# Performance work log

Hardware: AMD Instinct MI355X
Metric: run time of the kernel (lower is better)

Reference implementation:

```python
import jax, jax.numpy as jnp
import numpy as np

NUM_STEPS = 151            # num_steps from __init__
STEP = 2.0 / (NUM_STEPS - 1)
HALF = (NUM_STEPS - 1) // 2  # bin offset: t_j = -1 + j*STEP, 1/STEP = HALF
N = 4096
D = 512
NUM_CLASSES = 751


def _soft_histogram(s, mask, size):
    # Triangular-kernel (linear) soft binning, equivalent to the original
    # indsa/indsb masked-repeat construction: each similarity s in
    # [t_{j-1}, t_j] contributes (1-frac) to bin j-1 and frac to bin j.
    x = s / STEP
    k = jnp.floor(x)           # zero-gradient, plays the role of s_repeat_floor
    frac = x - k               # (s - (t_j - STEP)) / STEP
    kI = k.astype(jnp.int32)
    idx_lo = jnp.clip(kI + HALF, 0, NUM_STEPS - 1)
    idx_hi = jnp.clip(kI + HALF + 1, 0, NUM_STEPS - 1)
    hist = jnp.zeros((NUM_STEPS,), dtype=s.dtype)
    hist = hist.at[idx_lo].add((1.0 - frac) * mask)
    hist = hist.at[idx_hi].add(frac * mask)
    return hist / size


def setup_inputs() -> dict:
    key = jax.random.key(0)
    kf, kc = jax.random.split(key)
    return {
        "features": jax.random.normal(kf, (N, D), dtype=jnp.float32),
        "classes": jax.random.randint(kc, (N,), 0, NUM_CLASSES, dtype=jnp.int32),
    }


def reference(features, classes):
    # L2Normalization
    f = features / jnp.linalg.norm(features, axis=1, keepdims=True)
    dists = f @ f.T                                   # [N, N] cosine sims
    iu, ju = np.triu_indices(features.shape[0], 1)    # static upper-tri pairs
    s = dists[iu, ju]                                 # [P] P = N(N-1)/2
    pos = (classes[iu] == classes[ju]).astype(s.dtype)
    neg = 1.0 - pos
    hist_pos = _soft_histogram(s, pos, jnp.sum(pos))
    hist_neg = _soft_histogram(s, neg, jnp.sum(neg))
    cdf_pos = jnp.cumsum(hist_pos)                    # tril-masked column sums == cumsum
    return jnp.sum(hist_neg * cdf_pos)
```

## Files before the change

kernel.cpp:

```cpp
#include <hip/hip_runtime.h>
#include <math.h>

#define N 4096
#define D 512
#define NUM_STEPS 151
#define HALF_BINS 75
#define INV_STEP 75.0f
#define NUM_CLASSES 751
#define P_TOTAL 8386560.0f

#define WS_SUM_ALL 0
#define WS_POS_CNT 1
#define WS_SUM_POS 2
#define WS_S_POS   3
#define WS_G_OFF   8
#define WS_LIST_OFF 1024
#define MAXP (1 << 18)
#define WS_FEAT_OFF (WS_LIST_OFF + MAXP)
#define WS_FEATB_OFF (WS_FEAT_OFF + N * D)
#define WS_IDX_OFF  (WS_FEATB_OFF + N * D / 2)
#define WS_OFFS_OFF (WS_IDX_OFF + N)
#define WS_POFF_OFF (WS_OFFS_OFF + NUM_CLASSES + 1)

typedef __bf16 bf16x8 __attribute__((ext_vector_type(8)));
typedef float floatx4 __attribute__((ext_vector_type(4)));

__device__ __forceinline__ void load_lds16(const void* g, void* s) {
    __builtin_amdgcn_global_load_lds(
        (const __attribute__((address_space(1))) void*)g,
        (__attribute__((address_space(3))) void*)s, 16, 0, 0);
}

__global__ __launch_bounds__(256) void k_normalize(const float* __restrict__ feat,
                                                   float* __restrict__ nf,
                                                   __bf16* __restrict__ nfb) {
    int row = blockIdx.x;
    int t = threadIdx.x;
    const float* fr = feat + (size_t)row * D;
    float a = fr[t];
    float b = fr[t + 256];
    float ss = a * a + b * b;
    for (int o = 32; o > 0; o >>= 1) ss += __shfl_down(ss, o, 64);
    __shared__ float wsum[4];
    int lane = t & 63, wid = t >> 6;
    if (lane == 0) wsum[wid] = ss;
    __syncthreads();
    float tot = wsum[0] + wsum[1] + wsum[2] + wsum[3];
    float inv = 1.0f / sqrtf(tot);
    float na = a * inv, nb = b * inv;
    nf[(size_t)row * D + t] = na;
    nf[(size_t)row * D + t + 256] = nb;
    nfb[(size_t)row * D + t] = (__bf16)na;
    nfb[(size_t)row * D + t + 256] = (__bf16)nb;
}

__global__ __launch_bounds__(256) void k_sort(const int* __restrict__ cls,
                                              int* __restrict__ rowIdx,
                                              int* __restrict__ offs,
                                              int* __restrict__ pairOffs,
                                              int* __restrict__ posCntOut) {
    __shared__ int hcnt[NUM_CLASSES];
    __shared__ int hoff[NUM_CLASSES];
    __shared__ int poff[NUM_CLASSES];
    __shared__ int wsumR[4], wsumP[4];
    int t = threadIdx.x;
    for (int c = t; c < NUM_CLASSES; c += 256) hcnt[c] = 0;
    __syncthreads();
    for (int n = t; n < N; n += 256) atomicAdd(&hcnt[cls[n]], 1);
    __syncthreads();

    int c0 = t * 3;
    int cntPreR[3], cntPreP[3];
    int myR = 0, myP = 0;
    #pragma unroll
    for (int k = 0; k < 3; ++k) {
        int c = c0 + k;
        int cnt = (c < NUM_CLASSES) ? hcnt[c] : 0;
        cntPreR[k] = myR; cntPreP[k] = myP;
        myR += cnt;
        myP += cnt * (cnt - 1) / 2;
    }
    int lane = t & 63, wv = t >> 6;
    int incR = myR, incP = myP;
    for (int o = 1; o < 64; o <<= 1) {
        int rr = __shfl_up(incR, o, 64);
        int pp = __shfl_up(incP, o, 64);
        if (lane >= o) { incR += rr; incP += pp; }
    }
    if (lane == 63) { wsumR[wv] = incR; wsumP[wv] = incP; }
    __syncthreads();
    int baseR = 0, baseP = 0;
    for (int w = 0; w < wv; ++w) { baseR += wsumR[w]; baseP += wsumP[w]; }
    int exR = baseR + incR - myR;
    int exP = baseP + incP - myP;
    #pragma unroll
    for (int k = 0; k < 3; ++k) {
        int c = c0 + k;
        if (c < NUM_CLASSES) { hoff[c] = exR + cntPreR[k]; poff[c] = exP + cntPreP[k]; }
    }
    __syncthreads();

    for (int c = t; c < NUM_CLASSES; c += 256) hcnt[c] = hoff[c];
    __syncthreads();
    for (int n = t; n < N; n += 256) {
        int p = atomicAdd(&hcnt[cls[n]], 1);
        rowIdx[p] = n;
    }
    for (int c = t; c < NUM_CLASSES; c += 256) { offs[c] = hoff[c]; pairOffs[c] = poff[c]; }
    if (t == 0) {
        int totR = wsumR[0] + wsumR[1] + wsumR[2] + wsumR[3];
        int totP = wsumP[0] + wsumP[1] + wsumP[2] + wsumP[3];
        offs[NUM_CLASSES] = totR;
        pairOffs[NUM_CLASSES] = totP;
        *posCntOut = totP;
    }
}

__global__ __launch_bounds__(256) void k_pospairs3(const float* __restrict__ nf,
                                                   const int* __restrict__ rowIdx,
                                                   const int* __restrict__ offs,
                                                   const int* __restrict__ pairOffs,
                                                   float* __restrict__ posS) {
    int c = blockIdx.x;
    int o0 = offs[c], o1 = offs[c + 1];
    int nc = o1 - o0;
    if (nc < 2) return;
    int nPairs = nc * (nc - 1) / 2;
    int pBase = pairOffs[c];
    int lane = threadIdx.x & 63;
    int wave = threadIdx.x >> 6;
    for (int p = wave; p < nPairs; p += 4) {
        int a = 0, rem = p;
        while (rem >= nc - 1 - a) { rem -= nc - 1 - a; ++a; }
        int b = a + 1 + rem;
        int ri = rowIdx[o0 + a], rj = rowIdx[o0 + b];
        const float4* x4 = (const float4*)(nf + (size_t)ri * D);
        const float4* y4 = (const float4*)(nf + (size_t)rj * D);
        float4 xa = x4[lane * 2], xb = x4[lane * 2 + 1];
        float4 ya = y4[lane * 2], yb = y4[lane * 2 + 1];
        float s = xa.x * ya.x + xa.y * ya.y + xa.z * ya.z + xa.w * ya.w
                + xb.x * yb.x + xb.y * yb.y + xb.z * yb.z + xb.w * yb.w;
        for (int o = 32; o > 0; o >>= 1) s += __shfl_down(s, o, 64);
        if (lane == 0) posS[pBase + p] = s;
    }
}

__global__ __launch_bounds__(256) void k_build_cdf(const float* __restrict__ posS,
                                                   const int* __restrict__ posCnt,
                                                   float* __restrict__ G,
                                                   float* __restrict__ sumPosOut,
                                                   float* __restrict__ sPosOut) {
    __shared__ float hist[NUM_STEPS];
    __shared__ float Gs[NUM_STEPS];
    int t = threadIdx.x;
    int C = *posCnt;
    if (C > MAXP) C = MAXP;
    for (int b = t; b < NUM_STEPS; b += 256) hist[b] = 0.f;
    __syncthreads();
    for (int p = t; p < C; p += 256) {
        float s = posS[p];
        float x = s * INV_STEP;
        float kf = floorf(x);
        float frac = x - kf;
        int kI = (int)kf;
        int lo = min(max(kI + HALF_BINS, 0), NUM_STEPS - 1);
        int hi = min(max(kI + HALF_BINS + 1, 0), NUM_STEPS - 1);
        atomicAdd(&hist[lo], 1.0f - frac);
        atomicAdd(&hist[hi], frac);
    }
    __syncthreads();
    if (t == 0) {
        float invC = (C > 0) ? (1.0f / (float)C) : 0.f;
        float acc = 0.f;
        for (int b = 0; b < NUM_STEPS; ++b) {
            acc += hist[b];
            Gs[b] = acc * invC;
        }
    }
    __syncthreads();
    for (int b = t; b < NUM_STEPS; b += 256) G[b] = Gs[b];
    float ps = 0.f;
    for (int p = t; p < C; p += 256) {
        float s = posS[p];
        float x = s * INV_STEP;
        float kf = floorf(x);
        float frac = x - kf;
        int kI = (int)kf;
        int lo = min(max(kI + HALF_BINS, 0), NUM_STEPS - 1);
        int hi = min(max(kI + HALF_BINS + 1, 0), NUM_STEPS - 1);
        ps += (1.f - frac) * Gs[lo] + frac * Gs[hi];
    }
    for (int o = 32; o > 0; o >>= 1) ps += __shfl_down(ps, o, 64);
    __shared__ float wsum[4];
    int lane = t & 63, wid = t >> 6;
    if (lane == 0) wsum[wid] = ps;
    __syncthreads();
    if (t == 0) {
        *sumPosOut = wsum[0] + wsum[1] + wsum[2] + wsum[3];
        *sPosOut = (float)C;
    }
}

#define TILES_1D 32

__global__ __launch_bounds__(256) void k_gram(const __bf16* __restrict__ nfb,
                                              const float* __restrict__ G,
                                              float* __restrict__ sumAll) {
    int bid = blockIdx.x;
    int ti = 0, rem = bid;
    while (rem >= TILES_1D - ti) { rem -= TILES_1D - ti; ++ti; }
    int tj = ti + rem;

    __shared__ __align__(16) __bf16 As[8 * 512];
    __shared__ __align__(16) __bf16 Bs[8 * 512];
    __shared__ float Gs[NUM_STEPS];

    int tid = threadIdx.x;
    for (int b = tid; b < NUM_STEPS; b += 256) Gs[b] = G[b];

    int lane = tid & 63;
    int wave = tid >> 6;
    int rowA0 = ti * 128, rowB0 = tj * 128;

    int fr2 = lane & 15, kc2 = lane >> 4;
    int pS0 = wave * 2, pS1 = wave * 2 + 1;
    const __bf16* gA0 = nfb + (size_t)(rowA0 + pS0 * 16 + fr2) * D + kc2 * 8;
    const __bf16* gA1 = nfb + (size_t)(rowA0 + pS1 * 16 + fr2) * D + kc2 * 8;
    const __bf16* gB0 = nfb + (size_t)(rowB0 + pS0 * 16 + fr2) * D + kc2 * 8;
    const __bf16* gB1 = nfb + (size_t)(rowB0 + pS1 * 16 + fr2) * D + kc2 * 8;
    __bf16* lA0 = &As[pS0 * 512];
    __bf16* lA1 = &As[pS1 * 512];
    __bf16* lB0 = &Bs[pS0 * 512];
    __bf16* lB1 = &Bs[pS1 * 512];

    int pbA = (wave >> 1) * 4;
    int pbB = (wave & 1) * 4;

    floatx4 acc[4][4] = {};

    for (int kb = 0; kb < D / 32; ++kb) {
        int kbase = kb * 32;
        load_lds16(gA0 + kbase, lA0);
        load_lds16(gA1 + kbase, lA1);
        load_lds16(gB0 + kbase, lB0);
        load_lds16(gB1 + kbase, lB1);
        __syncthreads();

        bf16x8 a[4], b[4];
        #pragma unroll
        for (int r = 0; r < 4; ++r)
            a[r] = *(const bf16x8*)(&As[(pbA + r) * 512 + lane * 8]);
        #pragma unroll
        for (int c = 0; c < 4; ++c)
            b[c] = *(const bf16x8*)(&Bs[(pbB + c) * 512 + lane * 8]);

        #pragma unroll
        for (int r = 0; r < 4; ++r)
            #pragma unroll
            for (int c = 0; c < 4; ++c)
                acc[r][c] = __builtin_amdgcn_mfma_f32_16x16x32_bf16(a[r], b[c], acc[r][c], 0, 0, 0);
        __syncthreads();
    }

    int crow = (lane >> 4) * 4;
    int ccol = lane & 15;
    int wm = pbA * 16, wn = pbB * 16;
    float gsum = 0.f;
    #pragma unroll
    for (int r = 0; r < 4; ++r) {
        #pragma unroll
        for (int c = 0; c < 4; ++c) {
            #pragma unroll
            for (int reg = 0; reg < 4; ++reg) {
                int gi = rowA0 + wm + r * 16 + crow + reg;
                int gj = rowB0 + wn + c * 16 + ccol;
                if (gi < gj) {
                    float s = acc[r][c][reg];
                    float x = s * INV_STEP;
                    float kf = floorf(x);
                    float frac = x - kf;
                    int kI = (int)kf;
                    int lo = min(max(kI + HALF_BINS, 0), NUM_STEPS - 1);
                    int hi = min(max(kI + HALF_BINS + 1, 0), NUM_STEPS - 1);
                    gsum += (1.f - frac) * Gs[lo] + frac * Gs[hi];
                }
            }
        }
    }
    for (int o = 32; o > 0; o >>= 1) gsum += __shfl_down(gsum, o, 64);
    __shared__ float wsum[4];
    if ((tid & 63) == 0) wsum[tid >> 6] = gsum;
    __syncthreads();
    if (tid == 0) atomicAdd(sumAll, wsum[0] + wsum[1] + wsum[2] + wsum[3]);
}

__global__ void k_final(const float* __restrict__ wsf, float* __restrict__ out) {
    float C = wsf[WS_S_POS];
    float sneg = P_TOTAL - C;
    out[0] = (wsf[WS_SUM_ALL] - wsf[WS_SUM_POS]) / sneg;
}

extern "C" void kernel_launch(void* const* d_in, const int* in_sizes, int n_in,
                              void* d_out, int out_size, void* d_ws, size_t ws_size,
                              hipStream_t stream) {
    const float* feat = (const float*)d_in[0];
    const int* cls = (const int*)d_in[1];
    float* out = (float*)d_out;
    float* wsf = (float*)d_ws;
    int* wsi = (int*)d_ws;

    hipMemsetAsync(d_ws, 0, 4096, stream);

    float* nf = wsf + WS_FEAT_OFF;
    __bf16* nfb = (__bf16*)(wsf + WS_FEATB_OFF);
    float* posS = wsf + WS_LIST_OFF;
    float* G = wsf + WS_G_OFF;
    int* rowIdx = wsi + WS_IDX_OFF;
    int* offs = wsi + WS_OFFS_OFF;
    int* pairOffs = wsi + WS_POFF_OFF;

    k_normalize<<<N, 256, 0, stream>>>(feat, nf, nfb);
    k_sort<<<1, 256, 0, stream>>>(cls, rowIdx, offs, pairOffs, wsi + WS_POS_CNT);
    k_pospairs3<<<NUM_CLASSES, 256, 0, stream>>>(nf, rowIdx, offs, pairOffs, posS);
    k_build_cdf<<<1, 256, 0, stream>>>(posS, wsi + WS_POS_CNT, G,
                                       wsf + WS_SUM_POS, wsf + WS_S_POS);
    int nTiles = TILES_1D * (TILES_1D + 1) / 2;
    k_gram<<<nTiles, 256, 0, stream>>>(nfb, G, wsf + WS_SUM_ALL);
    k_final<<<1, 1, 0, stream>>>(wsf, out);
}
```

Baseline: 166.6 us.

## Fuse normalize and sort, precompute pair list, deepen gram K tile, fold final

Merges normalization and class sorting into one launch, with an extra block that builds an explicit list of positive pair row indices. The positive-pair dot-product kernel then reads that list through a flat grid-stride loop and no longer decodes pair indices per class. The gram kernel now stages K=64 per LDS round, halving barrier count, and the final scalar is computed by the last tile through an atomic done counter, which removes the k_final launch. The single-thread-per-class pair enumeration in the sort block may be serial and slow for large classes.

```diff
diff --git a/kernel.cpp b/kernel.cpp
--- a/kernel.cpp
+++ b/kernel.cpp
@@ -8,19 +8,20 @@
 #define INV_STEP 75.0f
 #define NUM_CLASSES 751
 #define P_TOTAL 8386560.0f
+#define TILES_1D 32
+#define NTILES (TILES_1D * (TILES_1D + 1) / 2)
 
 #define WS_SUM_ALL 0
 #define WS_POS_CNT 1
 #define WS_SUM_POS 2
 #define WS_S_POS   3
+#define WS_DONE    4
 #define WS_G_OFF   8
 #define WS_LIST_OFF 1024
 #define MAXP (1 << 18)
-#define WS_FEAT_OFF (WS_LIST_OFF + MAXP)
+#define WS_PAIR_OFF (WS_LIST_OFF + MAXP)
+#define WS_FEAT_OFF (WS_PAIR_OFF + 2 * MAXP)
 #define WS_FEATB_OFF (WS_FEAT_OFF + N * D)
-#define WS_IDX_OFF  (WS_FEATB_OFF + N * D / 2)
-#define WS_OFFS_OFF (WS_IDX_OFF + N)
-#define WS_POFF_OFF (WS_OFFS_OFF + NUM_CLASSES + 1)
 
 typedef __bf16 bf16x8 __attribute__((ext_vector_type(8)));
 typedef float floatx4 __attribute__((ext_vector_type(4)));
@@ -31,39 +32,42 @@
         (__attribute__((address_space(3))) void*)s, 16, 0, 0);
 }
 
-__global__ __launch_bounds__(256) void k_normalize(const float* __restrict__ feat,
-                                                   float* __restrict__ nf,
-                                                   __bf16* __restrict__ nfb) {
-    int row = blockIdx.x;
+__global__ __launch_bounds__(256) void k_prep(const float* __restrict__ feat,
+                                              const int* __restrict__ cls,
+                                              float* __restrict__ nf,
+                                              __bf16* __restrict__ nfb,
+                                              int2* __restrict__ pairRows,
+                                              int* __restrict__ posCntOut,
+                                              float* __restrict__ sPosOut) {
+    __shared__ int shmem[NUM_CLASSES * 3 + N / 4];
+    __shared__ int wsumR[4], wsumP[4];
+    __shared__ float wsumF[4];
     int t = threadIdx.x;
-    const float* fr = feat + (size_t)row * D;
-    float a = fr[t];
-    float b = fr[t + 256];
-    float ss = a * a + b * b;
-    for (int o = 32; o > 0; o >>= 1) ss += __shfl_down(ss, o, 64);
-    __shared__ float wsum[4];
-    int lane = t & 63, wid = t >> 6;
-    if (lane == 0) wsum[wid] = ss;
-    __syncthreads();
-    float tot = wsum[0] + wsum[1] + wsum[2] + wsum[3];
-    float inv = 1.0f / sqrtf(tot);
-    float na = a * inv, nb = b * inv;
-    nf[(size_t)row * D + t] = na;
-    nf[(size_t)row * D + t + 256] = nb;
-    nfb[(size_t)row * D + t] = (__bf16)na;
-    nfb[(size_t)row * D + t + 256] = (__bf16)nb;
-}
-
-__global__ __launch_bounds__(256) void k_sort(const int* __restrict__ cls,
-                                              int* __restrict__ rowIdx,
-                                              int* __restrict__ offs,
-                                              int* __restrict__ pairOffs,
-                                              int* __restrict__ posCntOut) {
-    __shared__ int hcnt[NUM_CLASSES];
-    __shared__ int hoff[NUM_CLASSES];
-    __shared__ int poff[NUM_CLASSES];
-    __shared__ int wsumR[4], wsumP[4];
-    int t = threadIdx.x;
+
+    if (blockIdx.x < N) {
+        int row = blockIdx.x;
+        const float* fr = feat + (size_t)row * D;
+        float a = fr[t];
+        float b = fr[t + 256];
+        float ss = a * a + b * b;
+        for (int o = 32; o > 0; o >>= 1) ss += __shfl_down(ss, o, 64);
+        int lane = t & 63, wid = t >> 6;
+        if (lane == 0) wsumF[wid] = ss;
+        __syncthreads();
+        float tot = wsumF[0] + wsumF[1] + wsumF[2] + wsumF[3];
+        float inv = 1.0f / sqrtf(tot);
+        float na = a * inv, nb = b * inv;
+        nf[(size_t)row * D + t] = na;
+        nf[(size_t)row * D + t + 256] = nb;
+        nfb[(size_t)row * D + t] = (__bf16)na;
+        nfb[(size_t)row * D + t + 256] = (__bf16)nb;
+        return;
+    }
+
+    int* hcnt = shmem;
+    int* hoff = shmem + NUM_CLASSES;
+    int* poff = shmem + 2 * NUM_CLASSES;
+    __shared__ int rowIdxL[N / 2];
     for (int c = t; c < NUM_CLASSES; c += 256) hcnt[c] = 0;
     __syncthreads();
     for (int n = t; n < N; n += 256) atomicAdd(&hcnt[cls[n]], 1);
@@ -104,52 +108,61 @@
     __syncthreads();
     for (int n = t; n < N; n += 256) {
         int p = atomicAdd(&hcnt[cls[n]], 1);
-        rowIdx[p] = n;
-    }
-    for (int c = t; c < NUM_CLASSES; c += 256) { offs[c] = hoff[c]; pairOffs[c] = poff[c]; }
+        int word = p >> 1, sh = (p & 1) * 16;
+        atomicAnd(&rowIdxL[word], ~(0xFFFF << sh));
+        atomicOr(&rowIdxL[word], (n & 0xFFFF) << sh);
+    }
+    __syncthreads();
+
+    for (int c = t; c < NUM_CLASSES; c += 256) {
+        int o0 = hoff[c];
+        int nc = (c + 1 < NUM_CLASSES ? hoff[c + 1]
+                                      : wsumR[0] + wsumR[1] + wsumR[2] + wsumR[3]) - o0;
+        int pb = poff[c];
+        int idx = 0;
+        for (int a = 0; a < nc - 1; ++a) {
+            int sa = o0 + a;
+            int ra = (rowIdxL[sa >> 1] >> ((sa & 1) * 16)) & 0xFFFF;
+            for (int b = a + 1; b < nc; ++b) {
+                int sb = o0 + b;
+                int rb = (rowIdxL[sb >> 1] >> ((sb & 1) * 16)) & 0xFFFF;
+                pairRows[pb + idx] = make_int2(ra, rb);
+                ++idx;
+            }
+        }
+    }
     if (t == 0) {
-        int totR = wsumR[0] + wsumR[1] + wsumR[2] + wsumR[3];
         int totP = wsumP[0] + wsumP[1] + wsumP[2] + wsumP[3];
-        offs[NUM_CLASSES] = totR;
-        pairOffs[NUM_CLASSES] = totP;
         *posCntOut = totP;
-    }
-}
-
-__global__ __launch_bounds__(256) void k_pospairs3(const float* __restrict__ nf,
-                                                   const int* __restrict__ rowIdx,
-                                                   const int* __restrict__ offs,
-                                                   const int* __restrict__ pairOffs,
+        *sPosOut = (float)totP;
+    }
+}
+
+__global__ __launch_bounds__(256) void k_pospairs4(const float* __restrict__ nf,
+                                                   const int2* __restrict__ pairRows,
+                                                   const int* __restrict__ posCnt,
                                                    float* __restrict__ posS) {
-    int c = blockIdx.x;
-    int o0 = offs[c], o1 = offs[c + 1];
-    int nc = o1 - o0;
-    if (nc < 2) return;
-    int nPairs = nc * (nc - 1) / 2;
-    int pBase = pairOffs[c];
+    int nP = *posCnt;
+    if (nP > MAXP) nP = MAXP;
+    int gw = (blockIdx.x * 256 + threadIdx.x) >> 6;
     int lane = threadIdx.x & 63;
-    int wave = threadIdx.x >> 6;
-    for (int p = wave; p < nPairs; p += 4) {
-        int a = 0, rem = p;
-        while (rem >= nc - 1 - a) { rem -= nc - 1 - a; ++a; }
-        int b = a + 1 + rem;
-        int ri = rowIdx[o0 + a], rj = rowIdx[o0 + b];
-        const float4* x4 = (const float4*)(nf + (size_t)ri * D);
-        const float4* y4 = (const float4*)(nf + (size_t)rj * D);
+    for (int p = gw; p < nP; p += 4096) {
+        int2 pr = pairRows[p];
+        const float4* x4 = (const float4*)(nf + (size_t)pr.x * D);
+        const float4* y4 = (const float4*)(nf + (size_t)pr.y * D);
         float4 xa = x4[lane * 2], xb = x4[lane * 2 + 1];
         float4 ya = y4[lane * 2], yb = y4[lane * 2 + 1];
         float s = xa.x * ya.x + xa.y * ya.y + xa.z * ya.z + xa.w * ya.w
                 + xb.x * yb.x + xb.y * yb.y + xb.z * yb.z + xb.w * yb.w;
         for (int o = 32; o > 0; o >>= 1) s += __shfl_down(s, o, 64);
-        if (lane == 0) posS[pBase + p] = s;
+        if (lane == 0) posS[p] = s;
     }
 }
 
 __global__ __launch_bounds__(256) void k_build_cdf(const float* __restrict__ posS,
                                                    const int* __restrict__ posCnt,
                                                    float* __restrict__ G,
-                                                   float* __restrict__ sumPosOut,
-                                                   float* __restrict__ sPosOut) {
+                                                   float* __restrict__ sumPosOut) {
     __shared__ float hist[NUM_STEPS];
     __shared__ float Gs[NUM_STEPS];
     int t = threadIdx.x;
@@ -195,24 +208,22 @@
     int lane = t & 63, wid = t >> 6;
     if (lane == 0) wsum[wid] = ps;
     __syncthreads();
-    if (t == 0) {
-        *sumPosOut = wsum[0] + wsum[1] + wsum[2] + wsum[3];
-        *sPosOut = (float)C;
-    }
-}
-
-#define TILES_1D 32
+    if (t == 0) *sumPosOut = wsum[0] + wsum[1] + wsum[2] + wsum[3];
+}
 
 __global__ __launch_bounds__(256) void k_gram(const __bf16* __restrict__ nfb,
                                               const float* __restrict__ G,
-                                              float* __restrict__ sumAll) {
+                                              float* __restrict__ sumAll,
+                                              const float* __restrict__ wsf,
+                                              int* __restrict__ done,
+                                              float* __restrict__ out) {
     int bid = blockIdx.x;
     int ti = 0, rem = bid;
     while (rem >= TILES_1D - ti) { rem -= TILES_1D - ti; ++ti; }
     int tj = ti + rem;
 
-    __shared__ __align__(16) __bf16 As[8 * 512];
-    __shared__ __align__(16) __bf16 Bs[8 * 512];
+    __shared__ __align__(16) __bf16 As[16 * 512];
+    __shared__ __align__(16) __bf16 Bs[16 * 512];
     __shared__ float Gs[NUM_STEPS];
 
     int tid = threadIdx.x;
@@ -223,42 +234,49 @@
     int rowA0 = ti * 128, rowB0 = tj * 128;
 
     int fr2 = lane & 15, kc2 = lane >> 4;
-    int pS0 = wave * 2, pS1 = wave * 2 + 1;
-    const __bf16* gA0 = nfb + (size_t)(rowA0 + pS0 * 16 + fr2) * D + kc2 * 8;
-    const __bf16* gA1 = nfb + (size_t)(rowA0 + pS1 * 16 + fr2) * D + kc2 * 8;
-    const __bf16* gB0 = nfb + (size_t)(rowB0 + pS0 * 16 + fr2) * D + kc2 * 8;
-    const __bf16* gB1 = nfb + (size_t)(rowB0 + pS1 * 16 + fr2) * D + kc2 * 8;
-    __bf16* lA0 = &As[pS0 * 512];
-    __bf16* lA1 = &As[pS1 * 512];
-    __bf16* lB0 = &Bs[pS0 * 512];
-    __bf16* lB1 = &Bs[pS1 * 512];
+    const __bf16* gA[4];
+    const __bf16* gB[4];
+    __bf16* lA[4];
+    __bf16* lB[4];
+    #pragma unroll
+    for (int i = 0; i < 4; ++i) {
+        int pid = wave * 4 + i;
+        int rp = pid >> 1, kc = pid & 1;
+        gA[i] = nfb + (size_t)(rowA0 + rp * 16 + fr2) * D + kc * 32 + kc2 * 8;
+        gB[i] = nfb + (size_t)(rowB0 + rp * 16 + fr2) * D + kc * 32 + kc2 * 8;
+        lA[i] = &As[pid * 512];
+        lB[i] = &Bs[pid * 512];
+    }
 
     int pbA = (wave >> 1) * 4;
     int pbB = (wave & 1) * 4;
 
     floatx4 acc[4][4] = {};
 
-    for (int kb = 0; kb < D / 32; ++kb) {
-        int kbase = kb * 32;
-        load_lds16(gA0 + kbase, lA0);
-        load_lds16(gA1 + kbase, lA1);
-        load_lds16(gB0 + kbase, lB0);
-        load_lds16(gB1 + kbase, lB1);
+    for (int kb = 0; kb < D / 64; ++kb) {
+        int kbase = kb * 64;
+        #pragma unroll
+        for (int i = 0; i < 4; ++i) {
+            load_lds16(gA[i] + kbase, lA[i]);
+            load_lds16(gB[i] + kbase, lB[i]);
+        }
         __syncthreads();
 
-        bf16x8 a[4], b[4];
         #pragma unroll
-        for (int r = 0; r < 4; ++r)
-            a[r] = *(const bf16x8*)(&As[(pbA + r) * 512 + lane * 8]);
-        #pragma unroll
-        for (int c = 0; c < 4; ++c)
-            b[c] = *(const bf16x8*)(&Bs[(pbB + c) * 512 + lane * 8]);
-
-        #pragma unroll
-        for (int r = 0; r < 4; ++r)
+        for (int kc = 0; kc < 2; ++kc) {
+            bf16x8 a[4], b[4];
+            #pragma unroll
+            for (int r = 0; r < 4; ++r)
+                a[r] = *(const bf16x8*)(&As[((pbA + r) * 2 + kc) * 512 + lane * 8]);
             #pragma unroll
             for (int c = 0; c < 4; ++c)
-                acc[r][c] = __builtin_amdgcn_mfma_f32_16x16x32_bf16(a[r], b[c], acc[r][c], 0, 0, 0);
+                b[c] = *(const bf16x8*)(&Bs[((pbB + c) * 2 + kc) * 512 + lane * 8]);
+            #pragma unroll
+            for (int r = 0; r < 4; ++r)
+                #pragma unroll
+                for (int c = 0; c < 4; ++c)
+                    acc[r][c] = __builtin_amdgcn_mfma_f32_16x16x32_bf16(a[r], b[c], acc[r][c], 0, 0, 0);
+        }
         __syncthreads();
     }
 
@@ -291,13 +309,17 @@
     __shared__ float wsum[4];
     if ((tid & 63) == 0) wsum[tid >> 6] = gsum;
     __syncthreads();
-    if (tid == 0) atomicAdd(sumAll, wsum[0] + wsum[1] + wsum[2] + wsum[3]);
-}
-
-__global__ void k_final(const float* __restrict__ wsf, float* __restrict__ out) {
-    float C = wsf[WS_S_POS];
-    float sneg = P_TOTAL - C;
-    out[0] = (wsf[WS_SUM_ALL] - wsf[WS_SUM_POS]) / sneg;
+    if (tid == 0) {
+        atomicAdd(sumAll, wsum[0] + wsum[1] + wsum[2] + wsum[3]);
+        __threadfence();
+        int d = atomicAdd(done, 1);
+        if (d == NTILES - 1) {
+            float sAll = atomicAdd(sumAll, 0.0f);
+            float sPos = wsf[WS_SUM_POS];
+            float C = wsf[WS_S_POS];
+            out[0] = (sAll - sPos) / (P_TOTAL - C);
+        }
+    }
 }
 
 extern "C" void kernel_launch(void* const* d_in, const int* in_sizes, int n_in,
@@ -314,17 +336,13 @@
     float* nf = wsf + WS_FEAT_OFF;
     __bf16* nfb = (__bf16*)(wsf + WS_FEATB_OFF);
     float* posS = wsf + WS_LIST_OFF;
+    int2* pairRows = (int2*)(wsi + WS_PAIR_OFF);
     float* G = wsf + WS_G_OFF;
-    int* rowIdx = wsi + WS_IDX_OFF;
-    int* offs = wsi + WS_OFFS_OFF;
-    int* pairOffs = wsi + WS_POFF_OFF;
-
-    k_normalize<<<N, 256, 0, stream>>>(feat, nf, nfb);
-    k_sort<<<1, 256, 0, stream>>>(cls, rowIdx, offs, pairOffs, wsi + WS_POS_CNT);
-    k_pospairs3<<<NUM_CLASSES, 256, 0, stream>>>(nf, rowIdx, offs, pairOffs, posS);
-    k_build_cdf<<<1, 256, 0, stream>>>(posS, wsi + WS_POS_CNT, G,
-                                       wsf + WS_SUM_POS, wsf + WS_S_POS);
-    int nTiles = TILES_1D * (TILES_1D + 1) / 2;
-    k_gram<<<nTiles, 256, 0, stream>>>(nfb, G, wsf + WS_SUM_ALL);
-    k_final<<<1, 1, 0, stream>>>(wsf, out);
-}
+
+    k_prep<<<N + 1, 256, 0, stream>>>(feat, cls, nf, nfb, pairRows,
+                                      wsi + WS_POS_CNT, wsf + WS_S_POS);
+    k_pospairs4<<<1024, 256, 0, stream>>>(nf, pairRows, wsi + WS_POS_CNT, posS);
+    k_build_cdf<<<1, 256, 0, stream>>>(posS, wsi + WS_POS_CNT, G, wsf + WS_SUM_POS);
+    k_gram<<<NTILES, 256, 0, stream>>>(nfb, G, wsf + WS_SUM_ALL, wsf,
+                                       wsi + WS_DONE, out);
+}
```

New measurement: 184.8 us. 1.11x slower.
